# Optimization experiments

Hardware: AMD Instinct MI355X
Metric: run time of the kernel (lower is better)

The kernel has to match this reference:

```python
import jax, jax.numpy as jnp
import numpy as np

GROUPS = 16          # fc_dim == groups
DIM_Q = 1024         # dim[0] == dim[1]
DIM_OUT = 1024       # dim[2]
DG = DIM_Q // GROUPS # per-group query/key dim = 64
EPS = 1e-6


def setup_inputs() -> dict:
    key = jax.random.key(0)
    ks = jax.random.split(key, 8)
    B, N, M, F, E = 2, 1024, 1024, 1024, 64
    std = 0.01
    return {
        "roi_feat": jax.random.normal(ks[0], (B, N, F), jnp.float32),
        "position_embedding": jax.random.uniform(ks[1], (B, N, M, E), jnp.float32),
        "pos_w": jax.random.normal(ks[2], (GROUPS, E), jnp.float32),  # nn.init.normal_ default std=1
        "pos_b": jnp.zeros((GROUPS,), jnp.float32),
        "q_w": jax.random.normal(ks[3], (DIM_Q, F), jnp.float32) * std,
        "q_b": jnp.zeros((DIM_Q,), jnp.float32),
        "k_w": jax.random.normal(ks[4], (DIM_Q, F), jnp.float32) * std,
        "k_b": jnp.zeros((DIM_Q,), jnp.float32),
        # grouped 1x1 conv: weight (out_ch=DIM_OUT, in_per_group=feat_dim) with groups=fc_dim
        "conv_w": jax.random.normal(ks[5], (DIM_OUT, F), jnp.float32) * std,
        "conv_b": jnp.zeros((DIM_OUT,), jnp.float32),
    }


def reference(roi_feat, position_embedding, pos_w, pos_b, q_w, q_b, k_w, k_b, conv_w, conv_b):
    B, N, F = roi_feat.shape
    M = position_embedding.shape[2]
    G, dg = GROUPS, DG

    nongt = roi_feat[:, :M, :]                                   # (B, M, F)

    # position bias: (B, N, M, G) -> (B, N, G, M)
    aff_w = jax.nn.relu(jnp.einsum('bnme,ge->bnmg', position_embedding, pos_w) + pos_b)
    aff_w = jnp.swapaxes(aff_w, 2, 3)                            # (B, N, G, M)

    q = (jnp.einsum('bnf,qf->bnq', roi_feat, q_w) + q_b).reshape(B, N, G, dg)
    k = (jnp.einsum('bmf,qf->bmq', nongt, k_w) + k_b).reshape(B, M, G, dg)

    # scaled dot-product per group: (B, N, G, M)
    aff = jnp.einsum('bngd,bmgd->bngm', q, k) * (1.0 / np.sqrt(dg))

    weighted = jnp.log(jnp.maximum(aff_w, EPS)) + aff            # (B, N, G, M)
    p = jax.nn.softmax(weighted, axis=-1)                        # (B, N, G, M)

    # weighted sum of values: (B, N, G, F)
    out_t = jnp.einsum('bngm,bmf->bngf', p, nongt)

    # grouped 1x1 conv: channels ordered group-major (N*G flatten -> G*F channels)
    cw = conv_w.reshape(G, DIM_OUT // G, F)                      # (G, out_per_group, F)
    out = jnp.einsum('bngf,gof->bngo', out_t, cw).reshape(B, N, DIM_OUT) + conv_b
    return out
```

## Files before the change

kernel.cpp:

```cpp
#include <hip/hip_runtime.h>

typedef unsigned short ushort_t;
typedef __attribute__((ext_vector_type(8))) short bf16x8;
typedef __attribute__((ext_vector_type(4))) float f32x4;

__device__ __forceinline__ unsigned short f2bf(float f) {
  unsigned int u = __float_as_uint(f);
  u += 0x7fffu + ((u >> 16) & 1u);
  return (unsigned short)(u >> 16);
}

__device__ __forceinline__ f32x4 mfma16(bf16x8 a, bf16x8 b, f32x4 c) {
  return __builtin_amdgcn_mfma_f32_16x16x32_bf16(a, b, c, 0, 0, 0);
}

__global__ void cvt_bf16_kernel(const float* __restrict__ src,
                                ushort_t* __restrict__ dst, int n) {
  int i = blockIdx.x * 256 + threadIdx.x;
  if (i < n) dst[i] = f2bf(src[i]);
}

__global__ __launch_bounds__(256) void gemm_bt(
    const ushort_t* __restrict__ A, const ushort_t* __restrict__ B,
    void* __restrict__ Cv, const float* __restrict__ bias,
    int lda, int ldb, int ldc,
    long sAb, long sAg, long sBb, long sBg, long sCb, long sCg,
    int K, float scale, int c_bf16) {
  int wave = threadIdx.x >> 6, lane = threadIdx.x & 63;
  int la = lane & 15, qd = lane >> 4;
  int z = blockIdx.z, b = z >> 4, g = z & 15;
  const ushort_t* Az = A + (long)b * sAb + (long)g * sAg;
  const ushort_t* Bz = B + (long)b * sBb + (long)g * sBg;
  int row0 = blockIdx.y * 64 + wave * 16;
  int col0 = blockIdx.x * 16;
  const ushort_t* ar = Az + (long)(row0 + la) * lda + qd * 8;
  const ushort_t* br = Bz + (long)(col0 + la) * ldb + qd * 8;
  f32x4 acc = {0.f, 0.f, 0.f, 0.f};
  for (int k = 0; k < K; k += 32) {
    bf16x8 av = *(const bf16x8*)(ar + k);
    bf16x8 bv = *(const bf16x8*)(br + k);
    acc = mfma16(av, bv, acc);
  }
  int crow = row0 + qd * 4, ccol = col0 + la;
  float bb = bias ? bias[ccol] : 0.f;
  long cbase = (long)b * sCb + (long)g * sCg;
#pragma unroll
  for (int j = 0; j < 4; ++j) {
    float v = acc[j] * scale + bb;
    long addr = cbase + (long)(crow + j) * ldc + ccol;
    if (c_bf16) ((ushort_t*)Cv)[addr] = f2bf(v);
    else ((float*)Cv)[addr] = v;
  }
}

__global__ __launch_bounds__(256) void pe_bias_kernel(
    const float* __restrict__ pe, const ushort_t* __restrict__ poswb,
    const float* __restrict__ pos_b, float* __restrict__ S) {
  int wave = threadIdx.x >> 6, lane = threadIdx.x & 63;
  int la = lane & 15, qd = lane >> 4;
  long r0 = ((long)blockIdx.x * 4 + wave) * 16;
  const ushort_t* ar = poswb + la * 64 + qd * 8;
  bf16x8 a0 = *(const bf16x8*)(ar);
  bf16x8 a1 = *(const bf16x8*)(ar + 32);
  long r = r0 + la;
  const float* prow = pe + r * 64 + qd * 8;
  f32x4 f0 = *(const f32x4*)(prow);
  f32x4 f1 = *(const f32x4*)(prow + 4);
  f32x4 f2 = *(const f32x4*)(prow + 32);
  f32x4 f3 = *(const f32x4*)(prow + 36);
  bf16x8 b0, b1;
#pragma unroll
  for (int j = 0; j < 4; ++j) {
    b0[j] = (short)f2bf(f0[j]); b0[j + 4] = (short)f2bf(f1[j]);
    b1[j] = (short)f2bf(f2[j]); b1[j + 4] = (short)f2bf(f3[j]);
  }
  f32x4 acc = {0.f, 0.f, 0.f, 0.f};
  acc = mfma16(a0, b0, acc);
  acc = mfma16(a1, b1, acc);
  long rr = r0 + la;
  long sbase = (rr >> 10) * 16384 + (rr & 1023);
#pragma unroll
  for (int j = 0; j < 4; ++j) {
    int g = qd * 4 + j;
    float w = __logf(fmaxf(acc[j] + pos_b[g], 1e-6f));
    long addr = sbase + (long)g * 1024;
    S[addr] += w;
  }
}

__global__ __launch_bounds__(256) void row_stats_kernel(
    const float* __restrict__ S, float* __restrict__ Mx,
    float* __restrict__ invL) {
  int wave = threadIdx.x >> 6, lane = threadIdx.x & 63;
  int rr = blockIdx.x * 4 + wave;
  const float* row = S + (long)rr * 1024;
  float mx = -3.0e38f, sm = 0.f;
#pragma unroll
  for (int i = 0; i < 16; ++i) {
    float v = row[lane + i * 64];
    if (v > mx) { sm *= __expf(mx - v); mx = v; }
    sm += __expf(v - mx);
  }
  for (int off = 32; off >= 1; off >>= 1) {
    float omx = __shfl_xor(mx, off);
    float osm = __shfl_xor(sm, off);
    float nmx = fmaxf(mx, omx);
    sm = sm * __expf(mx - nmx) + osm * __expf(omx - nmx);
    mx = nmx;
  }
  if (lane == 0) { Mx[rr] = mx; invL[rr] = 1.0f / sm; }
}

__global__ __launch_bounds__(256) void out_gemm_kernel(
    const float* __restrict__ S, const float* __restrict__ Mx,
    const float* __restrict__ invL, const ushort_t* __restrict__ V2T,
    const float* __restrict__ conv_b, float* __restrict__ out) {
  int wave = threadIdx.x >> 6, lane = threadIdx.x & 63;
  int la = lane & 15, qd = lane >> 4;
  int z = blockIdx.z, b = z >> 4, g = z & 15;
  int row0 = blockIdx.y * 16;
  int col0 = wave * 16;
  const float* Az = S + (long)b * 16777216 + (long)g * 1024;
  const ushort_t* Bz = V2T + (long)z * 65536;
  int an = row0 + la;
  const float* arow = Az + (long)an * 16384 + qd * 8;
  int rr = (b * 1024 + an) * 16 + g;
  float mx = Mx[rr], il = invL[rr];
  const ushort_t* brow = Bz + (long)(col0 + la) * 1024 + qd * 8;
  f32x4 acc = {0.f, 0.f, 0.f, 0.f};
  for (int k = 0; k < 1024; k += 32) {
    f32x4 f0 = *(const f32x4*)(arow + k);
    f32x4 f1 = *(const f32x4*)(arow + k + 4);
    bf16x8 av;
#pragma unroll
    for (int j = 0; j < 4; ++j) {
      av[j]     = (short)f2bf(__expf(f0[j] - mx) * il);
      av[j + 4] = (short)f2bf(__expf(f1[j] - mx) * il);
    }
    bf16x8 bv = *(const bf16x8*)(brow + k);
    acc = mfma16(av, bv, acc);
  }
  int crow = row0 + qd * 4, ccol = col0 + la;
  float cb = conv_b[g * 64 + ccol];
#pragma unroll
  for (int j = 0; j < 4; ++j) {
    out[(long)b * 1048576 + (long)(crow + j) * 1024 + g * 64 + ccol] =
        acc[j] + cb;
  }
}

extern "C" void kernel_launch(void* const* d_in, const int* in_sizes, int n_in,
                              void* d_out, int out_size, void* d_ws, size_t ws_size,
                              hipStream_t stream) {
  const float* roi_feat = (const float*)d_in[0];
  const float* pe       = (const float*)d_in[1];
  const float* pos_w    = (const float*)d_in[2];
  const float* pos_b    = (const float*)d_in[3];
  const float* q_w      = (const float*)d_in[4];
  const float* q_b      = (const float*)d_in[5];
  const float* k_w      = (const float*)d_in[6];
  const float* k_b      = (const float*)d_in[7];
  const float* conv_w   = (const float*)d_in[8];
  const float* conv_b   = (const float*)d_in[9];
  float* out = (float*)d_out;

  char* w = (char*)d_ws;
  ushort_t* rfb   = (ushort_t*)w; w += (size_t)4 << 20;
  ushort_t* qwb   = (ushort_t*)w; w += (size_t)2 << 20;
  ushort_t* kwb   = (ushort_t*)w; w += (size_t)2 << 20;
  ushort_t* cwb   = (ushort_t*)w; w += (size_t)2 << 20;
  ushort_t* poswb = (ushort_t*)w; w += (size_t)1 << 12;
  ushort_t* Qb    = (ushort_t*)w; w += (size_t)4 << 20;
  ushort_t* Kb    = (ushort_t*)w; w += (size_t)4 << 20;
  ushort_t* V2T   = (ushort_t*)w; w += (size_t)4 << 20;
  float*    Mx    = (float*)w;    w += (size_t)1 << 17;
  float*    invL  = (float*)w;    w += (size_t)1 << 17;
  float*    S     = (float*)w;    w += (size_t)134217728;

  cvt_bf16_kernel<<<8192, 256, 0, stream>>>(roi_feat, rfb, 2097152);
  cvt_bf16_kernel<<<4096, 256, 0, stream>>>(q_w, qwb, 1048576);
  cvt_bf16_kernel<<<4096, 256, 0, stream>>>(k_w, kwb, 1048576);
  cvt_bf16_kernel<<<4096, 256, 0, stream>>>(conv_w, cwb, 1048576);
  cvt_bf16_kernel<<<4, 256, 0, stream>>>(pos_w, poswb, 1024);

  gemm_bt<<<dim3(64, 32, 1), 256, 0, stream>>>(
      rfb, qwb, Qb, q_b, 1024, 1024, 1024, 0, 0, 0, 0, 0, 0, 1024, 1.f, 1);
  gemm_bt<<<dim3(64, 32, 1), 256, 0, stream>>>(
      rfb, kwb, Kb, k_b, 1024, 1024, 1024, 0, 0, 0, 0, 0, 0, 1024, 1.f, 1);
  gemm_bt<<<dim3(64, 1, 32), 256, 0, stream>>>(
      cwb, rfb, V2T, (const float*)nullptr, 1024, 1024, 1024,
      0, 65536, 1048576, 0, 1048576, 65536, 1024, 1.f, 1);
  gemm_bt<<<dim3(64, 16, 32), 256, 0, stream>>>(
      Qb, Kb, S, (const float*)nullptr, 1024, 1024, 16384,
      1048576, 64, 1048576, 64, 16777216, 1024, 64, 0.125f, 0);
  pe_bias_kernel<<<32768, 256, 0, stream>>>(pe, poswb, pos_b, S);
  row_stats_kernel<<<8192, 256, 0, stream>>>(S, Mx, invL);
  out_gemm_kernel<<<dim3(1, 64, 32), 256, 0, stream>>>(
      S, Mx, invL, V2T, conv_b, out);
}
```

Measured before the change: 1.100 ms.

## Fuse QK scores, position bias, softmax and value GEMM into flash-style kernel

Replaces the four-stage pipeline (QK GEMM into a 128MB fp32 score buffer, position-bias add, row stats, output GEMM) with one online-softmax kernel. Each block handles 8 query rows for all 16 groups. It stages a tile of the position embedding in LDS, computes the log-bias there, and streams K and V tiles with running max and sum. This removes several full read/write passes over the huge score tensor. The cost is low parallelism (256 blocks, with MFMA tiles half-wasted on 8 rows) and extra syncs per tile.

```diff
diff --git a/kernel.cpp b/kernel.cpp
--- a/kernel.cpp
+++ b/kernel.cpp
@@ -53,99 +53,136 @@
   }
 }
 
-__global__ __launch_bounds__(256) void pe_bias_kernel(
+__global__ __launch_bounds__(1024, 4) void flash_kernel(
     const float* __restrict__ pe, const ushort_t* __restrict__ poswb,
-    const float* __restrict__ pos_b, float* __restrict__ S) {
-  int wave = threadIdx.x >> 6, lane = threadIdx.x & 63;
+    const float* __restrict__ pos_b, const ushort_t* __restrict__ Qb,
+    const ushort_t* __restrict__ Kb, const ushort_t* __restrict__ V2T,
+    const float* __restrict__ conv_b, float* __restrict__ out) {
+  __shared__ ushort_t peb[256 * 72];
+  __shared__ float    wlog[256 * 17];
+  __shared__ ushort_t ptrb[16][8 * 32];
+
+  int tid = threadIdx.x;
+  int wave = tid >> 6, lane = tid & 63;
   int la = lane & 15, qd = lane >> 4;
-  long r0 = ((long)blockIdx.x * 4 + wave) * 16;
-  const ushort_t* ar = poswb + la * 64 + qd * 8;
-  bf16x8 a0 = *(const bf16x8*)(ar);
-  bf16x8 a1 = *(const bf16x8*)(ar + 32);
-  long r = r0 + la;
-  const float* prow = pe + r * 64 + qd * 8;
-  f32x4 f0 = *(const f32x4*)(prow);
-  f32x4 f1 = *(const f32x4*)(prow + 4);
-  f32x4 f2 = *(const f32x4*)(prow + 32);
-  f32x4 f3 = *(const f32x4*)(prow + 36);
-  bf16x8 b0, b1;
-#pragma unroll
-  for (int j = 0; j < 4; ++j) {
-    b0[j] = (short)f2bf(f0[j]); b0[j + 4] = (short)f2bf(f1[j]);
-    b1[j] = (short)f2bf(f2[j]); b1[j + 4] = (short)f2bf(f3[j]);
-  }
-  f32x4 acc = {0.f, 0.f, 0.f, 0.f};
-  acc = mfma16(a0, b0, acc);
-  acc = mfma16(a1, b1, acc);
-  long rr = r0 + la;
-  long sbase = (rr >> 10) * 16384 + (rr & 1023);
-#pragma unroll
-  for (int j = 0; j < 4; ++j) {
-    int g = qd * 4 + j;
-    float w = __logf(fmaxf(acc[j] + pos_b[g], 1e-6f));
-    long addr = sbase + (long)g * 1024;
-    S[addr] += w;
-  }
-}
-
-__global__ __launch_bounds__(256) void row_stats_kernel(
-    const float* __restrict__ S, float* __restrict__ Mx,
-    float* __restrict__ invL) {
-  int wave = threadIdx.x >> 6, lane = threadIdx.x & 63;
-  int rr = blockIdx.x * 4 + wave;
-  const float* row = S + (long)rr * 1024;
-  float mx = -3.0e38f, sm = 0.f;
-#pragma unroll
-  for (int i = 0; i < 16; ++i) {
-    float v = row[lane + i * 64];
-    if (v > mx) { sm *= __expf(mx - v); mx = v; }
-    sm += __expf(v - mx);
-  }
-  for (int off = 32; off >= 1; off >>= 1) {
-    float omx = __shfl_xor(mx, off);
-    float osm = __shfl_xor(sm, off);
-    float nmx = fmaxf(mx, omx);
-    sm = sm * __expf(mx - nmx) + osm * __expf(omx - nmx);
-    mx = nmx;
-  }
-  if (lane == 0) { Mx[rr] = mx; invL[rr] = 1.0f / sm; }
-}
-
-__global__ __launch_bounds__(256) void out_gemm_kernel(
-    const float* __restrict__ S, const float* __restrict__ Mx,
-    const float* __restrict__ invL, const ushort_t* __restrict__ V2T,
-    const float* __restrict__ conv_b, float* __restrict__ out) {
-  int wave = threadIdx.x >> 6, lane = threadIdx.x & 63;
-  int la = lane & 15, qd = lane >> 4;
-  int z = blockIdx.z, b = z >> 4, g = z & 15;
-  int row0 = blockIdx.y * 16;
-  int col0 = wave * 16;
-  const float* Az = S + (long)b * 16777216 + (long)g * 1024;
-  const ushort_t* Bz = V2T + (long)z * 65536;
-  int an = row0 + la;
-  const float* arow = Az + (long)an * 16384 + qd * 8;
-  int rr = (b * 1024 + an) * 16 + g;
-  float mx = Mx[rr], il = invL[rr];
-  const ushort_t* brow = Bz + (long)(col0 + la) * 1024 + qd * 8;
-  f32x4 acc = {0.f, 0.f, 0.f, 0.f};
-  for (int k = 0; k < 1024; k += 32) {
-    f32x4 f0 = *(const f32x4*)(arow + k);
-    f32x4 f1 = *(const f32x4*)(arow + k + 4);
-    bf16x8 av;
+  int g = wave;
+  int bx = blockIdx.x;
+  int b = bx & 1, nt = bx >> 1;
+  int n0 = nt * 8;
+
+  const ushort_t* qptr =
+      Qb + (((long)(b * 1024 + n0 + (la & 7))) << 10) + g * 64 + qd * 8;
+  bf16x8 aq0 = *(const bf16x8*)qptr;
+  bf16x8 aq1 = *(const bf16x8*)(qptr + 32);
+  const ushort_t* pwp = poswb + la * 64 + qd * 8;
+  bf16x8 pw0 = *(const bf16x8*)pwp;
+  bf16x8 pw1 = *(const bf16x8*)(pwp + 32);
+  float pb_la = pos_b[la];
+
+  int n_l = tid >> 7, rr = tid & 127;
+  int m_l = rr >> 2, e0 = (rr & 3) * 16;
+  const float* psrc =
+      pe + (((long)(b * 1024 + n0 + n_l) << 10) + m_l) * 64 + e0;
+  int pebidx = (n_l * 32 + m_l) * 72 + e0;
+
+  f32x4 O0 = {0,0,0,0}, O1 = {0,0,0,0}, O2 = {0,0,0,0}, O3 = {0,0,0,0};
+  float m_i[4], l_i[4];
+#pragma unroll
+  for (int j = 0; j < 4; ++j) { m_i[j] = -1e30f; l_i[j] = 0.f; }
+
+  f32x4 p0 = *(const f32x4*)(psrc);
+  f32x4 p1 = *(const f32x4*)(psrc + 4);
+  f32x4 p2 = *(const f32x4*)(psrc + 8);
+  f32x4 p3 = *(const f32x4*)(psrc + 12);
+
+  for (int t = 0; t < 32; ++t) {
+    bf16x8 c0, c1;
 #pragma unroll
     for (int j = 0; j < 4; ++j) {
-      av[j]     = (short)f2bf(__expf(f0[j] - mx) * il);
-      av[j + 4] = (short)f2bf(__expf(f1[j] - mx) * il);
-    }
-    bf16x8 bv = *(const bf16x8*)(brow + k);
-    acc = mfma16(av, bv, acc);
-  }
-  int crow = row0 + qd * 4, ccol = col0 + la;
-  float cb = conv_b[g * 64 + ccol];
-#pragma unroll
-  for (int j = 0; j < 4; ++j) {
-    out[(long)b * 1048576 + (long)(crow + j) * 1024 + g * 64 + ccol] =
-        acc[j] + cb;
+      c0[j] = (short)f2bf(p0[j]); c0[j + 4] = (short)f2bf(p1[j]);
+      c1[j] = (short)f2bf(p2[j]); c1[j + 4] = (short)f2bf(p3[j]);
+    }
+    *(bf16x8*)&peb[pebidx] = c0;
+    *(bf16x8*)&peb[pebidx + 8] = c1;
+    __syncthreads();
+    if (t < 31) {
+      const float* ps = psrc + (t + 1) * 2048;
+      p0 = *(const f32x4*)(ps);
+      p1 = *(const f32x4*)(ps + 4);
+      p2 = *(const f32x4*)(ps + 8);
+      p3 = *(const f32x4*)(ps + 12);
+    }
+    const ushort_t* pa = &peb[(wave * 16 + la) * 72 + qd * 8];
+    bf16x8 wa0 = *(const bf16x8*)pa;
+    bf16x8 wa1 = *(const bf16x8*)(pa + 32);
+    f32x4 wacc = {0.f, 0.f, 0.f, 0.f};
+    wacc = mfma16(wa0, pw0, wacc);
+    wacc = mfma16(wa1, pw1, wacc);
+    int wrow = wave * 16 + qd * 4;
+#pragma unroll
+    for (int j = 0; j < 4; ++j)
+      wlog[(wrow + j) * 17 + la] = __logf(fmaxf(wacc[j] + pb_la, 1e-6f));
+    __syncthreads();
+    int m0 = t * 32;
+    const ushort_t* kbase =
+        Kb + (((long)(b * 1024 + m0)) << 10) + g * 64 + qd * 8;
+    bf16x8 kb0 = *(const bf16x8*)(kbase + (long)la * 1024);
+    bf16x8 kb1 = *(const bf16x8*)(kbase + (long)la * 1024 + 32);
+    bf16x8 kb2 = *(const bf16x8*)(kbase + (long)(la + 16) * 1024);
+    bf16x8 kb3 = *(const bf16x8*)(kbase + (long)(la + 16) * 1024 + 32);
+    const ushort_t* vb = V2T + ((long)(b * 16 + g) << 16) + m0 + qd * 8;
+    bf16x8 v0 = *(const bf16x8*)(vb + (long)la * 1024);
+    bf16x8 v1 = *(const bf16x8*)(vb + (long)(16 + la) * 1024);
+    bf16x8 v2 = *(const bf16x8*)(vb + (long)(32 + la) * 1024);
+    bf16x8 v3 = *(const bf16x8*)(vb + (long)(48 + la) * 1024);
+    f32x4 s0 = {0.f, 0.f, 0.f, 0.f}, s1 = {0.f, 0.f, 0.f, 0.f};
+    s0 = mfma16(aq0, kb0, s0); s0 = mfma16(aq1, kb1, s0);
+    s1 = mfma16(aq0, kb2, s1); s1 = mfma16(aq1, kb3, s1);
+#pragma unroll
+    for (int j = 0; j < 4; ++j) {
+      int nl = (qd * 4 + j) & 7;
+      float sv0 = s0[j] * 0.125f + wlog[(nl * 32 + la) * 17 + g];
+      float sv1 = s1[j] * 0.125f + wlog[(nl * 32 + la + 16) * 17 + g];
+      float mrow = fmaxf(sv0, sv1);
+      mrow = fmaxf(mrow, __shfl_xor(mrow, 1));
+      mrow = fmaxf(mrow, __shfl_xor(mrow, 2));
+      mrow = fmaxf(mrow, __shfl_xor(mrow, 4));
+      mrow = fmaxf(mrow, __shfl_xor(mrow, 8));
+      float mn = fmaxf(m_i[j], mrow);
+      float alpha = __expf(m_i[j] - mn);
+      m_i[j] = mn;
+      float e0v = __expf(sv0 - mn), e1v = __expf(sv1 - mn);
+      float ps = e0v + e1v;
+      ps += __shfl_xor(ps, 1); ps += __shfl_xor(ps, 2);
+      ps += __shfl_xor(ps, 4); ps += __shfl_xor(ps, 8);
+      l_i[j] = l_i[j] * alpha + ps;
+      O0[j] *= alpha; O1[j] *= alpha; O2[j] *= alpha; O3[j] *= alpha;
+      if (qd < 2) {
+        int row = qd * 4 + j;
+        ptrb[wave][row * 32 + la] = f2bf(e0v);
+        ptrb[wave][row * 32 + la + 16] = f2bf(e1v);
+      }
+    }
+    bf16x8 pA = *(const bf16x8*)&ptrb[wave][(la & 7) * 32 + qd * 8];
+    O0 = mfma16(pA, v0, O0);
+    O1 = mfma16(pA, v1, O1);
+    O2 = mfma16(pA, v2, O2);
+    O3 = mfma16(pA, v3, O3);
+  }
+
+  if (qd < 2) {
+    float* ob = out + (((long)(b * 1024 + n0)) << 10) + g * 64 + la;
+    const float* cb = conv_b + g * 64 + la;
+#pragma unroll
+    for (int j = 0; j < 4; ++j) {
+      int row = qd * 4 + j;
+      float il = 1.0f / l_i[j];
+      float* orow = ob + ((long)row << 10);
+      orow[0]  = O0[j] * il + cb[0];
+      orow[16] = O1[j] * il + cb[16];
+      orow[32] = O2[j] * il + cb[32];
+      orow[48] = O3[j] * il + cb[48];
+    }
   }
 }
 
@@ -173,9 +210,6 @@
   ushort_t* Qb    = (ushort_t*)w; w += (size_t)4 << 20;
   ushort_t* Kb    = (ushort_t*)w; w += (size_t)4 << 20;
   ushort_t* V2T   = (ushort_t*)w; w += (size_t)4 << 20;
-  float*    Mx    = (float*)w;    w += (size_t)1 << 17;
-  float*    invL  = (float*)w;    w += (size_t)1 << 17;
-  float*    S     = (float*)w;    w += (size_t)134217728;
 
   cvt_bf16_kernel<<<8192, 256, 0, stream>>>(roi_feat, rfb, 2097152);
   cvt_bf16_kernel<<<4096, 256, 0, stream>>>(q_w, qwb, 1048576);
@@ -190,11 +224,7 @@
   gemm_bt<<<dim3(64, 1, 32), 256, 0, stream>>>(
       cwb, rfb, V2T, (const float*)nullptr, 1024, 1024, 1024,
       0, 65536, 1048576, 0, 1048576, 65536, 1024, 1.f, 1);
-  gemm_bt<<<dim3(64, 16, 32), 256, 0, stream>>>(
-      Qb, Kb, S, (const float*)nullptr, 1024, 1024, 16384,
-      1048576, 64, 1048576, 64, 16777216, 1024, 64, 0.125f, 0);
-  pe_bias_kernel<<<32768, 256, 0, stream>>>(pe, poswb, pos_b, S);
-  row_stats_kernel<<<8192, 256, 0, stream>>>(S, Mx, invL);
-  out_gemm_kernel<<<dim3(1, 64, 32), 256, 0, stream>>>(
-      S, Mx, invL, V2T, conv_b, out);
-}
+
+  flash_kernel<<<256, 1024, 0, stream>>>(
+      pe, poswb, pos_b, Qb, Kb, V2T, conv_b, out);
+}
```

Measured after the change: 1.008 ms. 8.3% less time.
